# Optimization experiments

Measured on AMD Instinct MI355X. Metric: run time of the kernel, lower is better.

Reference implementation:

```python
import jax, jax.numpy as jnp
import numpy as np

B, S, D, H, INNER = 2, 2048, 1024, 16, 4096
HD = D // H
EPS = 1e-5


def setup_inputs() -> dict:
    key = jax.random.key(0)
    ks = jax.random.split(key, 8)

    def w(k, o, i):
        return jax.random.normal(k, (o, i), jnp.float32) * 0.02

    return {
        "hidden_states": jax.random.normal(ks[0], (B, S, D), jnp.float32),
        "attention_mask": jnp.ones((B, S), jnp.float32),
        "wq": w(ks[1], D, D), "bq": jnp.zeros((D,), jnp.float32),
        "wk": w(ks[2], D, D), "bk": jnp.zeros((D,), jnp.float32),
        "wv": w(ks[3], D, D), "bv": jnp.zeros((D,), jnp.float32),
        "wo": w(ks[4], D, D), "bo": jnp.zeros((D,), jnp.float32),
        "w1": w(ks[5], INNER, D), "b1": jnp.zeros((INNER,), jnp.float32),
        "w2": w(ks[6], D, INNER), "b2": jnp.zeros((D,), jnp.float32),
        "g1": jnp.ones((D,), jnp.float32), "be1": jnp.zeros((D,), jnp.float32),
        "g2": jnp.ones((D,), jnp.float32), "be2": jnp.zeros((D,), jnp.float32),
        "w_bits": 8,
        "a_bits": 8,
    }


def fake_quant(x, bits):
    # symmetric per-tensor fake quantization with straight-through estimator
    qmax = 2.0 ** (bits - 1) - 1.0
    scale = jnp.maximum(jnp.max(jnp.abs(x)), 1e-8) / qmax
    q = jnp.round(jnp.clip(x / scale, -qmax, qmax)) * scale
    return x + jax.lax.stop_gradient(q - x)


def qlinear(x, w, b, w_bits, a_bits):
    return fake_quant(x, a_bits) @ fake_quant(w, w_bits).T + b


def layernorm(x, g, b):
    m = jnp.mean(x, axis=-1, keepdims=True)
    v = jnp.mean((x - m) ** 2, axis=-1, keepdims=True)
    return (x - m) * jax.lax.rsqrt(v + EPS) * g + b


def reference(hidden_states, attention_mask, wq, bq, wk, bk, wv, bv, wo, bo,
              w1, b1, w2, b2, g1, be1, g2, be2, w_bits, a_bits):
    # --- attention sub-block ---
    residual = hidden_states
    x = layernorm(hidden_states, g1, be1)
    q = qlinear(x, wq, bq, w_bits, a_bits).reshape(B, S, H, HD)
    k = qlinear(x, wk, bk, w_bits, a_bits).reshape(B, S, H, HD)
    v = qlinear(x, wv, bv, w_bits, a_bits).reshape(B, S, H, HD)
    scores = jnp.einsum("bqhd,bkhd->bhqk", q, k) / jnp.sqrt(jnp.float32(HD))
    scores = scores + (1.0 - attention_mask)[:, None, None, :] * -10000.0
    probs = jax.nn.softmax(scores, axis=-1)
    attn = jnp.einsum("bhqk,bkhd->bqhd", probs, v).reshape(B, S, D)
    attn = qlinear(attn, wo, bo, w_bits, a_bits)
    hidden = residual + attn
    # --- MLP sub-block ---
    residual = hidden
    x = layernorm(hidden, g2, be2)
    x = qlinear(x, w1, b1, w_bits, a_bits)
    x = jax.nn.gelu(x, approximate=False)
    x = qlinear(x, w2, b2, w_bits, a_bits)
    return residual + x
```

## Files before the change

### kernel.cpp

```cpp
#include <hip/hip_runtime.h>
#include <hip/hip_bf16.h>
#include <math.h>

typedef __bf16 bf16;
typedef signed char i8;
typedef __bf16 bf16x8 __attribute__((ext_vector_type(8)));
typedef __bf16 bf16x4 __attribute__((ext_vector_type(4)));
typedef signed char i8x4 __attribute__((ext_vector_type(4)));
typedef signed char i8x8 __attribute__((ext_vector_type(8)));
typedef int    i32x4 __attribute__((ext_vector_type(4)));
typedef float  f32x4  __attribute__((ext_vector_type(4)));
typedef float  f32x16 __attribute__((ext_vector_type(16)));
typedef unsigned int u32x4 __attribute__((ext_vector_type(4)));

static constexpr int B_  = 2;
static constexpr int S_  = 2048;
static constexpr int D_  = 1024;
static constexpr int H_  = 16;
static constexpr int HD_ = 64;
static constexpr int I_  = 4096;
static constexpr int NT  = B_ * S_;

__device__ __forceinline__ void atomicMaxF(float* p, float v) {
  atomicMax((unsigned int*)p, __float_as_uint(v));
}

__device__ __forceinline__ f32x16 mfma32(bf16x8 a, bf16x8 b, f32x16 c) {
  return __builtin_amdgcn_mfma_f32_32x32x16_bf16(a, b, c, 0, 0, 0);
}

__device__ __forceinline__ i32x4 mfma_i8(i32x4 a, i32x4 b, i32x4 c) {
  return __builtin_amdgcn_mfma_i32_16x16x64_i8(a, b, c, 0, 0, 0);
}

__device__ __forceinline__ void gload16(const void* g, void* lds) {
  __builtin_amdgcn_global_load_lds(
      (const __attribute__((address_space(1))) void*)g,
      (__attribute__((address_space(3))) void*)lds, 16, 0, 0);
}

__device__ __forceinline__ float quant1(float x, float scale, float qmax) {
  return rintf(fminf(fmaxf(x / scale, -qmax), qmax)) * scale;
}
__device__ __forceinline__ i8 quantn(float x, float scale, float qmax) {
  return (i8)(int)rintf(fminf(fmaxf(x / scale, -qmax), qmax));
}

__device__ __forceinline__ void stage64b(const bf16* __restrict__ g, int rs, bf16* lds, int t) {
  #pragma unroll
  for (int r = 0; r < 4; r++) {
    const int cl  = r * 128 + t;
    const int row = cl >> 3;
    const int scr = (cl & 7) ^ (row & 7);
    gload16(g + (size_t)row * rs + scr * 8,
            (char*)lds + (size_t)(r * 128 + (t & 64)) * 16);
  }
}

__global__ __launch_bounds__(256) void k_prep(const float* __restrict__ mask,
                                              float* __restrict__ madd, float* __restrict__ scal) {
  constexpr float MSK2 = -14426.950408889634f;
  const int i = blockIdx.x * 256 + threadIdx.x;
  if (blockIdx.x == 0 && threadIdx.x < 32) scal[threadIdx.x] = 0.f;
  if (i < B_ * S_) madd[i] = (1.0f - mask[i]) * MSK2;
}

struct WArgs {
  const float* w[6];
  i8* q[6];
  size_t n4[6];
};

__global__ __launch_bounds__(256) void k_absmax6(WArgs a, float* __restrict__ slots) {
  const int z = blockIdx.z;
  const float* __restrict__ x = a.w[z];
  const size_t n4 = a.n4[z];
  size_t i = (size_t)blockIdx.x * 256 + threadIdx.x;
  const size_t stride = (size_t)gridDim.x * 256;
  float m = 0.f;
  for (; i < n4; i += stride) {
    float4 v = ((const float4*)x)[i];
    m = fmaxf(m, fmaxf(fmaxf(fabsf(v.x), fabsf(v.y)), fmaxf(fabsf(v.z), fabsf(v.w))));
  }
  #pragma unroll
  for (int o = 32; o; o >>= 1) m = fmaxf(m, __shfl_xor(m, o));
  __shared__ float red[4];
  if ((threadIdx.x & 63) == 0) red[threadIdx.x >> 6] = m;
  __syncthreads();
  if (threadIdx.x == 0)
    atomicMaxF(slots + z, fmaxf(fmaxf(red[0], red[1]), fmaxf(red[2], red[3])));
}

__global__ __launch_bounds__(256) void k_quant6(WArgs a, const float* __restrict__ slots,
                                                const int* __restrict__ bits) {
  const int z = blockIdx.z;
  const float* __restrict__ x = a.w[z];
  i8* __restrict__ y = a.q[z];
  const size_t n4 = a.n4[z];
  const float qmax  = (float)((1 << (*bits - 1)) - 1);
  const float scale = fmaxf(slots[z], 1e-8f) / qmax;
  size_t i = (size_t)blockIdx.x * 256 + threadIdx.x;
  const size_t stride = (size_t)gridDim.x * 256;
  for (; i < n4; i += stride) {
    float4 v = ((const float4*)x)[i];
    i8x4 o;
    o[0] = quantn(v.x, scale, qmax);
    o[1] = quantn(v.y, scale, qmax);
    o[2] = quantn(v.z, scale, qmax);
    o[3] = quantn(v.w, scale, qmax);
    ((i8x4*)y)[i] = o;
  }
}

__global__ __launch_bounds__(256) void k_quant(const float* __restrict__ x, i8* __restrict__ y,
                                               const float* __restrict__ slot,
                                               const int* __restrict__ bits, size_t n4) {
  const float qmax  = (float)((1 << (*bits - 1)) - 1);
  const float scale = fmaxf(*slot, 1e-8f) / qmax;
  size_t i = (size_t)blockIdx.x * 256 + threadIdx.x;
  const size_t stride = (size_t)gridDim.x * 256;
  for (; i < n4; i += stride) {
    float4 v = ((const float4*)x)[i];
    i8x4 o;
    o[0] = quantn(v.x, scale, qmax);
    o[1] = quantn(v.y, scale, qmax);
    o[2] = quantn(v.z, scale, qmax);
    o[3] = quantn(v.w, scale, qmax);
    ((i8x4*)y)[i] = o;
  }
}

__global__ __launch_bounds__(256) void k_qgelu(const bf16* __restrict__ x, i8* __restrict__ y,
                                               const float* __restrict__ slot,
                                               const int* __restrict__ bits, size_t n8) {
  const float qmax  = (float)((1 << (*bits - 1)) - 1);
  const float scale = fmaxf(*slot, 1e-8f) / qmax;
  size_t i = (size_t)blockIdx.x * 256 + threadIdx.x;
  if (i >= n8) return;
  bf16x8 v = ((const bf16x8*)x)[i];
  i8x8 o;
  #pragma unroll
  for (int j = 0; j < 8; j++) o[j] = quantn((float)v[j], scale, qmax);
  ((i8x8*)y)[i] = o;
}

__global__ __launch_bounds__(256) void k_ln(const float* __restrict__ x, const float* __restrict__ g,
                                            const float* __restrict__ be, float* __restrict__ y,
                                            float* __restrict__ slot) {
  const int row = blockIdx.x, t = threadIdx.x;
  const float4 v = ((const float4*)(x + (size_t)row * D_))[t];
  float s = v.x + v.y + v.z + v.w;
  float q = v.x * v.x + v.y * v.y + v.z * v.z + v.w * v.w;
  #pragma unroll
  for (int o = 32; o; o >>= 1) { s += __shfl_xor(s, o); q += __shfl_xor(q, o); }
  __shared__ float red[8];
  const int wid = t >> 6;
  if ((t & 63) == 0) { red[wid] = s; red[4 + wid] = q; }
  __syncthreads();
  s = red[0] + red[1] + red[2] + red[3];
  q = red[4] + red[5] + red[6] + red[7];
  const float mean = s * (1.f / D_);
  const float rstd = rsqrtf(q * (1.f / D_) - mean * mean + 1e-5f);
  const float4 gv = ((const float4*)g)[t];
  const float4 bv = ((const float4*)be)[t];
  float4 o;
  o.x = (v.x - mean) * rstd * gv.x + bv.x;
  o.y = (v.y - mean) * rstd * gv.y + bv.y;
  o.z = (v.z - mean) * rstd * gv.z + bv.z;
  o.w = (v.w - mean) * rstd * gv.w + bv.w;
  ((float4*)(y + (size_t)row * D_))[t] = o;
  float m = fmaxf(fmaxf(fabsf(o.x), fabsf(o.y)), fmaxf(fabsf(o.z), fabsf(o.w)));
  #pragma unroll
  for (int oo = 32; oo; oo >>= 1) m = fmaxf(m, __shfl_xor(m, oo));
  __syncthreads();
  if ((t & 63) == 0) red[wid] = m;
  __syncthreads();
  if (t == 0) atomicMaxF(slot, fmaxf(fmaxf(red[0], red[1]), fmaxf(red[2], red[3])));
}

struct GemmArgs {
  const i8* A;
  const i8* B0; const i8* B1; const i8* B2;
  const float* bias0; const float* bias1; const float* bias2;
  void* out0; void* out1; void* out2;
  const float* res;
  float* slot;
  const float* sa;
  const float* sw0; const float* sw1; const float* sw2;
  const int* abit; const int* wbit;
  int K; int ldc;
};

template <int MODE, int MT>
__device__ __forceinline__ void gemm_body(GemmArgs a, int bx, int by, int bz) {
  constexpr int TM = MT * 32;
  __shared__ __align__(16) i8 As[2][TM * 128];
  __shared__ __align__(16) i8 Bs[2][128 * 128];
  const int t = threadIdx.x, wid = t >> 6, lane = t & 63;
  const int grp = lane >> 4, l15 = lane & 15;
  const int wm = wid >> 1, wn = wid & 1;
  const size_t m0 = (size_t)bx * TM, n0 = (size_t)by * 128;
  const int K = a.K, ldc = a.ldc;

  const i8* Bw; const float* bias; void* outv; const float* swp;
  if constexpr (MODE == 0) {
    Bw   = bz == 0 ? a.B0 : (bz == 1 ? a.B1 : a.B2);
    bias = bz == 0 ? a.bias0 : (bz == 1 ? a.bias1 : a.bias2);
    outv = bz == 0 ? a.out0 : (bz == 1 ? a.out1 : a.out2);
    swp  = bz == 0 ? a.sw0 : (bz == 1 ? a.sw1 : a.sw2);
  } else {
    Bw = a.B0; bias = a.bias0; outv = a.out0; swp = a.sw0;
  }
  const float qa = (float)((1 << (*a.abit - 1)) - 1);
  const float qw = (float)((1 << (*a.wbit - 1)) - 1);
  const float sasw = (fmaxf(*a.sa, 1e-8f) / qa) * (fmaxf(*swp, 1e-8f) / qw);

  i32x4 acc[MT][4];
  #pragma unroll
  for (int m = 0; m < MT; m++)
    #pragma unroll
    for (int n = 0; n < 4; n++) acc[m][n] = i32x4{0, 0, 0, 0};

  auto stage = [&](int kt, int buf) {
    #pragma unroll
    for (int r = 0; r < MT; r++) {
      const int cl = r * 256 + t;
      const int row = cl >> 3, c = cl & 7;
      gload16(a.A + (m0 + row) * (size_t)K + kt + ((c ^ (row & 7)) * 16),
              (char*)&As[buf][0] + (size_t)(r * 256 + (t & 192)) * 16);
    }
    #pragma unroll
    for (int r = 0; r < 4; r++) {
      const int cl = r * 256 + t;
      const int row = cl >> 3, c = cl & 7;
      gload16(Bw + (n0 + row) * (size_t)K + kt + ((c ^ (row & 7)) * 16),
              (char*)&Bs[buf][0] + (size_t)(r * 256 + (t & 192)) * 16);
    }
  };

  stage(0, 0);
  __syncthreads();
  int cur = 0;
  for (int kt = 0; kt < K; kt += 128) {
    if (kt + 128 < K) stage(kt + 128, cur ^ 1);
    #pragma unroll
    for (int ks = 0; ks < 2; ks++) {
      i32x4 bfv[4];
      #pragma unroll
      for (int n = 0; n < 4; n++) {
        const int rb = wn * 64 + n * 16 + l15;
        bfv[n] = *(const i32x4*)(&Bs[cur][0] + rb * 128 + (((ks * 4 + grp) ^ (rb & 7)) * 16));
      }
      #pragma unroll
      for (int m = 0; m < MT; m++) {
        const int ra = wm * (MT * 16) + m * 16 + l15;
        const i32x4 af = *(const i32x4*)(&As[cur][0] + ra * 128 + (((ks * 4 + grp) ^ (ra & 7)) * 16));
        #pragma unroll
        for (int n = 0; n < 4; n++)
          acc[m][n] = mfma_i8(af, bfv[n], acc[m][n]);
      }
    }
    __syncthreads();
    cur ^= 1;
  }

  const size_t gr0 = m0 + wm * (MT * 16) + grp * 4;
  const size_t gc0 = n0 + wn * 64 + l15;

  if constexpr (MODE == 0) {
    if (bz == 2) {
      #pragma unroll
      for (int n = 0; n < 4; n++) {
        const size_t gc = gc0 + n * 16;
        const float bc = bias[gc];
        #pragma unroll
        for (int m = 0; m < MT; m++) {
          const size_t gr = gr0 + m * 16;
          const size_t bb = gr >> 11, s0 = gr & (S_ - 1);
          bf16x4 vv;
          #pragma unroll
          for (int i = 0; i < 4; i++) vv[i] = (bf16)((float)acc[m][n][i] * sasw + bc);
          *(bf16x4*)((bf16*)outv + bb * (size_t)D_ * S_ + gc * S_ + s0) = vv;
        }
      }
      return;
    }
  }

  float lmax = 0.f;
  #pragma unroll
  for (int n = 0; n < 4; n++) {
    const size_t gc = gc0 + n * 16;
    const float bc = bias[gc];
    #pragma unroll
    for (int m = 0; m < MT; m++) {
      const size_t gr = gr0 + m * 16;
      #pragma unroll
      for (int i = 0; i < 4; i++) {
        const float v = (float)acc[m][n][i] * sasw + bc;
        const size_t idx = (gr + i) * (size_t)ldc + gc;
        if constexpr (MODE == 0) {
          ((bf16*)outv)[idx] = (bf16)v;
        } else if constexpr (MODE == 1) {
          ((float*)outv)[idx] = v + a.res[idx];
        } else {
          const float gl = 0.5f * v * (1.0f + erff(v * 0.7071067811865475f));
          ((bf16*)outv)[idx] = (bf16)gl;
          lmax = fmaxf(lmax, fabsf(gl));
        }
      }
    }
  }
  if constexpr (MODE == 2) {
    #pragma unroll
    for (int o = 32; o; o >>= 1) lmax = fmaxf(lmax, __shfl_xor(lmax, o));
    float* red = (float*)&As[0][0];
    if (lane == 0) red[wid] = lmax;
    __syncthreads();
    if (t == 0) atomicMaxF(a.slot, fmaxf(fmaxf(red[0], red[1]), fmaxf(red[2], red[3])));
  }
}

__global__ __launch_bounds__(256) void k_gqkv(GemmArgs a) {
  const int d = blockIdx.x, c = d & 7, s = d >> 3;
  gemm_body<0, 4>(a, s / 3, c, s % 3);
}
__global__ __launch_bounds__(256) void k_gout(GemmArgs a) {
  const int d = blockIdx.x, c = d & 7, s = d >> 3;
  gemm_body<1, 2>(a, s, c, 0);
}
__global__ __launch_bounds__(256) void k_gmlp1(GemmArgs a) {
  const int d = blockIdx.x, c = d & 7, s = d >> 3;
  gemm_body<2, 4>(a, s >> 2, c * 4 + (s & 3), 0);
}
__global__ __launch_bounds__(256) void k_gmlp2(GemmArgs a) {
  const int d = blockIdx.x, c = d & 7, s = d >> 3;
  gemm_body<1, 2>(a, ((c >> 2) << 5) | (s >> 1), ((c & 3) << 1) | (s & 1), 0);
}

__global__ __launch_bounds__(128) void k_attn(const bf16* __restrict__ qb, const bf16* __restrict__ kb,
                                              const bf16* __restrict__ vt, const float* __restrict__ madd,
                                              float* __restrict__ out, float* __restrict__ slot) {
  constexpr float SCL2 = 0.18033688011112042f;
  constexpr float THR  = 8.0f;
  __shared__ __align__(16) bf16 Ks[2][64 * 64];
  __shared__ __align__(16) bf16 Vs[2][64 * 64];
  __shared__ float red[2];
  const int t = threadIdx.x, wid = t >> 6, lane = t & 63;
  const int l31 = lane & 31, hi = lane >> 5;
  const int b = blockIdx.y >> 4, h = blockIdx.y & 15;
  const size_t qkbase = ((size_t)b * S_) * D_ + (size_t)h * HD_;
  const size_t vtbase = (size_t)b * D_ * S_ + (size_t)h * HD_ * S_;
  const int q = blockIdx.x * 64 + wid * 32 + l31;

  bf16x8 qf[4];
  #pragma unroll
  for (int j = 0; j < 4; j++)
    qf[j] = *(const bf16x8*)(qb + qkbase + (size_t)q * D_ + j * 16 + hi * 8);

  f32x16 ao0, ao1;
  #pragma unroll
  for (int r = 0; r < 16; r++) { ao0[r] = 0.f; ao1[r] = 0.f; }
  float mi = -INFINITY, li = 0.f;

  stage64b(kb + qkbase, D_, Ks[0], t);
  stage64b(vt + vtbase, S_, Vs[0], t);
  __syncthreads();
  int cur = 0;

  const float* mp = madd + (size_t)b * S_ + hi * 4;

  for (int kt0 = 0; kt0 < S_; kt0 += 64) {
    f32x4 mv[2][4];
    #pragma unroll
    for (int kb2 = 0; kb2 < 2; kb2++)
      #pragma unroll
      for (int g = 0; g < 4; g++)
        mv[kb2][g] = *(const f32x4*)(mp + kt0 + kb2 * 32 + g * 8);
    __builtin_amdgcn_sched_barrier(0);
    if (kt0 + 64 < S_) {
      stage64b(kb + qkbase + (size_t)(kt0 + 64) * D_, D_, Ks[cur ^ 1], t);
      stage64b(vt + vtbase + (kt0 + 64), S_, Vs[cur ^ 1], t);
    }

    f32x16 s0, s1;
    #pragma unroll
    for (int r = 0; r < 16; r++) { s0[r] = 0.f; s1[r] = 0.f; }
    #pragma unroll
    for (int j = 0; j < 4; j++) {
      const int ch = (j * 2 + hi);
      const bf16x8 kf0 = *(const bf16x8*)(&Ks[cur][0] + l31 * 64 + ((ch ^ (l31 & 7)) * 8));
      const bf16x8 kf1 = *(const bf16x8*)(&Ks[cur][0] + (32 + l31) * 64 + ((ch ^ (l31 & 7)) * 8));
      s0 = mfma32(kf0, qf[j], s0);
      s1 = mfma32(kf1, qf[j], s1);
    }

    float pv_[32];
    #pragma unroll
    for (int r = 0; r < 16; r++) pv_[r]      = s0[r] * SCL2 + mv[0][r >> 2][r & 3];
    #pragma unroll
    for (int r = 0; r < 16; r++) pv_[16 + r] = s1[r] * SCL2 + mv[1][r >> 2][r & 3];

    float mx = pv_[0];
    #pragma unroll
    for (int r = 1; r < 32; r++) mx = fmaxf(mx, pv_[r]);
    mx = fmaxf(mx, __shfl_xor(mx, 32));

    if (!__all(mx - mi <= THR)) {
      const float mnew = fmaxf(mi, mx);
      const float co = exp2f(mi - mnew);
      li *= co;
      #pragma unroll
      for (int r = 0; r < 16; r++) { ao0[r] *= co; ao1[r] *= co; }
      mi = mnew;
    }

    float ls = 0.f;
    #pragma unroll
    for (int r = 0; r < 32; r++) { pv_[r] = exp2f(pv_[r] - mi); ls += pv_[r]; }
    li += ls;

    unsigned pk[16];
    #pragma unroll
    for (int tt = 0; tt < 8; tt++) {
      asm("v_cvt_pk_bf16_f32 %0, %1, %2" : "=v"(pk[tt])     : "v"(pv_[2 * tt]),      "v"(pv_[2 * tt + 1]));
      asm("v_cvt_pk_bf16_f32 %0, %1, %2" : "=v"(pk[8 + tt]) : "v"(pv_[16 + 2 * tt]), "v"(pv_[16 + 2 * tt + 1]));
    }
    #pragma unroll
    for (int g = 0; g < 4; g++) {
      asm volatile("v_permlane32_swap_b32 %0, %1" : "+v"(pk[4 * g]),     "+v"(pk[4 * g + 2]));
      asm volatile("v_permlane32_swap_b32 %0, %1" : "+v"(pk[4 * g + 1]), "+v"(pk[4 * g + 3]));
    }

    #pragma unroll
    for (int j = 0; j < 4; j++) {
      const u32x4 w = {pk[4 * j], pk[4 * j + 1], pk[4 * j + 2], pk[4 * j + 3]};
      const bf16x8 pf = __builtin_bit_cast(bf16x8, w);
      const int ch = (j * 2 + hi);
      const bf16x8 vf0 = *(const bf16x8*)(&Vs[cur][0] + l31 * 64 + ((ch ^ (l31 & 7)) * 8));
      const bf16x8 vf1 = *(const bf16x8*)(&Vs[cur][0] + (32 + l31) * 64 + ((ch ^ (l31 & 7)) * 8));
      ao0 = mfma32(vf0, pf, ao0);
      ao1 = mfma32(vf1, pf, ao1);
    }
    __syncthreads();
    cur ^= 1;
  }

  li += __shfl_xor(li, 32);
  const float invl = 1.0f / li;
  float lmax = 0.f;
  float* orow = out + qkbase + (size_t)q * D_;
  #pragma unroll
  for (int db2 = 0; db2 < 2; db2++) {
    #pragma unroll
    for (int rg = 0; rg < 4; rg++) {
      float4 o;
      o.x = (db2 ? ao1[rg * 4 + 0] : ao0[rg * 4 + 0]) * invl;
      o.y = (db2 ? ao1[rg * 4 + 1] : ao0[rg * 4 + 1]) * invl;
      o.z = (db2 ? ao1[rg * 4 + 2] : ao0[rg * 4 + 2]) * invl;
      o.w = (db2 ? ao1[rg * 4 + 3] : ao0[rg * 4 + 3]) * invl;
      *(float4*)(orow + db2 * 32 + rg * 8 + hi * 4) = o;
      lmax = fmaxf(lmax, fmaxf(fmaxf(fabsf(o.x), fabsf(o.y)), fmaxf(fabsf(o.z), fabsf(o.w))));
    }
  }
  #pragma unroll
  for (int o = 32; o; o >>= 1) lmax = fmaxf(lmax, __shfl_xor(lmax, o));
  if (lane == 0) red[wid] = lmax;
  __syncthreads();
  if (t == 0) atomicMaxF(slot, fmaxf(red[0], red[1]));
}

extern "C" void kernel_launch(void* const* d_in, const int* in_sizes, int n_in,
                              void* d_out, int out_size, void* d_ws, size_t ws_size,
                              hipStream_t stream) {
  const float* hs   = (const float*)d_in[0];
  const float* mask = (const float*)d_in[1];
  const float* wq = (const float*)d_in[2];  const float* bq = (const float*)d_in[3];
  const float* wk = (const float*)d_in[4];  const float* bk = (const float*)d_in[5];
  const float* wv = (const float*)d_in[6];  const float* bv = (const float*)d_in[7];
  const float* wo = (const float*)d_in[8];  const float* bo = (const float*)d_in[9];
  const float* w1 = (const float*)d_in[10]; const float* b1 = (const float*)d_in[11];
  const float* w2 = (const float*)d_in[12]; const float* b2 = (const float*)d_in[13];
  const float* g1 = (const float*)d_in[14]; const float* be1 = (const float*)d_in[15];
  const float* g2 = (const float*)d_in[16]; const float* be2 = (const float*)d_in[17];
  const int* wbits = (const int*)d_in[18];
  const int* abits = (const int*)d_in[19];

  char* ws = (char*)d_ws;
  size_t off = 0;
  float* scal = (float*)ws;                      off += 256;
  float* maddg= (float*)(ws + off);              off += (size_t)NT * 4;
  float* fbuf = (float*)(ws + off);              off += (size_t)NT * D_ * 4;
  i8*    qx   = (i8*)(ws + off);                 off += (size_t)NT * D_;
  bf16*  qb   = (bf16*)(ws + off);               off += (size_t)NT * D_ * 2;
  bf16*  kbuf = (bf16*)(ws + off);               off += (size_t)NT * D_ * 2;
  bf16*  vbuf = (bf16*)(ws + off);               off += (size_t)NT * D_ * 2;
  float* h2   = (float*)(ws + off);              off += (size_t)NT * D_ * 4;
  bf16*  h1   = (bf16*)(ws + off);               off += (size_t)NT * I_ * 2;
  i8*    h1q  = (i8*)(ws + off);                 off += (size_t)NT * I_;
  i8*    wqq  = (i8*)(ws + off);                 off += (size_t)D_ * D_;
  i8*    wkq  = (i8*)(ws + off);                 off += (size_t)D_ * D_;
  i8*    wvq  = (i8*)(ws + off);                 off += (size_t)D_ * D_;
  i8*    woq  = (i8*)(ws + off);                 off += (size_t)D_ * D_;
  i8*    w1q  = (i8*)(ws + off);                 off += (size_t)I_ * D_;
  i8*    w2q  = (i8*)(ws + off);                 off += (size_t)D_ * I_;
  if (ws_size < off) return;

  k_prep<<<NT / 256, 256, 0, stream>>>(mask, maddg, scal);

  const size_t nDD4 = (size_t)D_ * D_ / 4, nDI4 = (size_t)D_ * I_ / 4;
  WArgs wa;
  wa.w[0] = wq; wa.w[1] = wk; wa.w[2] = wv; wa.w[3] = wo; wa.w[4] = w1; wa.w[5] = w2;
  wa.q[0] = wqq; wa.q[1] = wkq; wa.q[2] = wvq; wa.q[3] = woq; wa.q[4] = w1q; wa.q[5] = w2q;
  wa.n4[0] = nDD4; wa.n4[1] = nDD4; wa.n4[2] = nDD4; wa.n4[3] = nDD4;
  wa.n4[4] = nDI4; wa.n4[5] = nDI4;
  k_absmax6<<<dim3(1024, 1, 6), 256, 0, stream>>>(wa, scal + 4);
  k_quant6<<<dim3(1024, 1, 6), 256, 0, stream>>>(wa, scal + 4, wbits);

  const size_t nND4 = (size_t)NT * D_ / 4;

  k_ln<<<NT, 256, 0, stream>>>(hs, g1, be1, fbuf, scal + 0);
  k_quant<<<2048, 256, 0, stream>>>(fbuf, qx, scal + 0, abits, nND4);
  {
    GemmArgs ga{};
    ga.A = qx; ga.B0 = wqq; ga.B1 = wkq; ga.B2 = wvq;
    ga.bias0 = bq; ga.bias1 = bk; ga.bias2 = bv;
    ga.out0 = qb; ga.out1 = kbuf; ga.out2 = vbuf;
    ga.sa = scal + 0; ga.sw0 = scal + 4; ga.sw1 = scal + 5; ga.sw2 = scal + 6;
    ga.abit = abits; ga.wbit = wbits;
    ga.K = D_; ga.ldc = D_;
    k_gqkv<<<(NT / 128) * (D_ / 128) * 3, 256, 0, stream>>>(ga);
  }

  k_attn<<<dim3(S_ / 64, B_ * H_), 128, 0, stream>>>(qb, kbuf, vbuf, maddg, fbuf, scal + 1);
  k_quant<<<2048, 256, 0, stream>>>(fbuf, qx, scal + 1, abits, nND4);
  {
    GemmArgs ga{};
    ga.A = qx; ga.B0 = woq; ga.bias0 = bo; ga.out0 = h2; ga.res = hs;
    ga.sa = scal + 1; ga.sw0 = scal + 7;
    ga.abit = abits; ga.wbit = wbits;
    ga.K = D_; ga.ldc = D_;
    k_gout<<<(NT / 64) * (D_ / 128), 256, 0, stream>>>(ga);
  }

  k_ln<<<NT, 256, 0, stream>>>(h2, g2, be2, fbuf, scal + 2);
  k_quant<<<2048, 256, 0, stream>>>(fbuf, qx, scal + 2, abits, nND4);
  {
    GemmArgs ga{};
    ga.A = qx; ga.B0 = w1q; ga.bias0 = b1; ga.out0 = h1; ga.slot = scal + 3;
    ga.sa = scal + 2; ga.sw0 = scal + 8;
    ga.abit = abits; ga.wbit = wbits;
    ga.K = D_; ga.ldc = I_;
    k_gmlp1<<<(NT / 128) * (I_ / 128), 256, 0, stream>>>(ga);
  }
  k_qgelu<<<(NT * (size_t)I_ / 8 + 255) / 256, 256, 0, stream>>>(h1, h1q, scal + 3, abits,
                                                                 (size_t)NT * I_ / 8);
  {
    GemmArgs ga{};
    ga.A = h1q; ga.B0 = w2q; ga.bias0 = b2; ga.out0 = d_out; ga.res = h2;
    ga.sa = scal + 3; ga.sw0 = scal + 9;
    ga.abit = abits; ga.wbit = wbits;
    ga.K = I_; ga.ldc = D_;
    k_gmlp2<<<(NT / 64) * (D_ / 128), 256, 0, stream>>>(ga);
  }
}
```

Baseline: 427.2 us.

## Split attention over KV halves with combine kernel; deepen GEMM prefetch pipeline

```diff
diff --git a/kernel.cpp b/kernel.cpp
--- a/kernel.cpp
+++ b/kernel.cpp
@@ -46,14 +46,14 @@
   return (i8)(int)rintf(fminf(fmaxf(x / scale, -qmax), qmax));
 }
 
-__device__ __forceinline__ void stage64b(const bf16* __restrict__ g, int rs, bf16* lds, int t) {
-  #pragma unroll
-  for (int r = 0; r < 4; r++) {
-    const int cl  = r * 128 + t;
+__device__ __forceinline__ void stage64(const bf16* __restrict__ g, int rs, bf16* lds, int tt) {
+  #pragma unroll
+  for (int r = 0; r < 2; r++) {
+    const int cl  = r * 256 + tt;
     const int row = cl >> 3;
     const int scr = (cl & 7) ^ (row & 7);
     gload16(g + (size_t)row * rs + scr * 8,
-            (char*)lds + (size_t)(r * 128 + (t & 64)) * 16);
+            (char*)lds + (size_t)(r * 256 + (tt & 192)) * 16);
   }
 }
 
@@ -194,6 +194,7 @@
 template <int MODE, int MT>
 __device__ __forceinline__ void gemm_body(GemmArgs a, int bx, int by, int bz) {
   constexpr int TM = MT * 32;
+  constexpr int NLOAD = MT + 4;
   __shared__ __align__(16) i8 As[2][TM * 128];
   __shared__ __align__(16) i8 Bs[2][128 * 128];
   const int t = threadIdx.x, wid = t >> 6, lane = t & 63;
@@ -211,9 +212,6 @@
   } else {
     Bw = a.B0; bias = a.bias0; outv = a.out0; swp = a.sw0;
   }
-  const float qa = (float)((1 << (*a.abit - 1)) - 1);
-  const float qw = (float)((1 << (*a.wbit - 1)) - 1);
-  const float sasw = (fmaxf(*a.sa, 1e-8f) / qa) * (fmaxf(*swp, 1e-8f) / qw);
 
   i32x4 acc[MT][4];
   #pragma unroll
@@ -239,10 +237,17 @@
   };
 
   stage(0, 0);
-  __syncthreads();
+  if (K > 128) stage(128, 1);
   int cur = 0;
   for (int kt = 0; kt < K; kt += 128) {
-    if (kt + 128 < K) stage(kt + 128, cur ^ 1);
+    if (kt + 128 < K) {
+      if constexpr (MT == 4) asm volatile("s_waitcnt vmcnt(8)" ::: "memory");
+      else                   asm volatile("s_waitcnt vmcnt(6)" ::: "memory");
+    } else {
+      asm volatile("s_waitcnt vmcnt(0)" ::: "memory");
+    }
+    __builtin_amdgcn_sched_barrier(0);
+    __builtin_amdgcn_s_barrier();
     #pragma unroll
     for (int ks = 0; ks < 2; ks++) {
       i32x4 bfv[4];
@@ -260,9 +265,14 @@
           acc[m][n] = mfma_i8(af, bfv[n], acc[m][n]);
       }
     }
-    __syncthreads();
+    __builtin_amdgcn_s_barrier();
+    if (kt + 256 < K) stage(kt + 256, cur);
     cur ^= 1;
   }
+
+  const float qa = (float)((1 << (*a.abit - 1)) - 1);
+  const float qw = (float)((1 << (*a.wbit - 1)) - 1);
+  const float sasw = (fmaxf(*a.sa, 1e-8f) / qa) * (fmaxf(*swp, 1e-8f) / qw);
 
   const size_t gr0 = m0 + wm * (MT * 16) + grp * 4;
   const size_t gc0 = n0 + wn * 64 + l15;
@@ -338,20 +348,21 @@
   gemm_body<1, 2>(a, ((c >> 2) << 5) | (s >> 1), ((c & 3) << 1) | (s & 1), 0);
 }
 
-__global__ __launch_bounds__(128) void k_attn(const bf16* __restrict__ qb, const bf16* __restrict__ kb,
+__global__ __launch_bounds__(256) void k_attn(const bf16* __restrict__ qb, const bf16* __restrict__ kb,
                                               const bf16* __restrict__ vt, const float* __restrict__ madd,
-                                              float* __restrict__ out, float* __restrict__ slot) {
+                                              float* __restrict__ pO, float* __restrict__ ml) {
   constexpr float SCL2 = 0.18033688011112042f;
   constexpr float THR  = 8.0f;
   __shared__ __align__(16) bf16 Ks[2][64 * 64];
   __shared__ __align__(16) bf16 Vs[2][64 * 64];
-  __shared__ float red[2];
   const int t = threadIdx.x, wid = t >> 6, lane = t & 63;
   const int l31 = lane & 31, hi = lane >> 5;
-  const int b = blockIdx.y >> 4, h = blockIdx.y & 15;
+  const int bh = blockIdx.y, b = bh >> 4, h = bh & 15;
+  const int z = blockIdx.z;
+  const int k0base = z * (S_ / 2);
   const size_t qkbase = ((size_t)b * S_) * D_ + (size_t)h * HD_;
   const size_t vtbase = (size_t)b * D_ * S_ + (size_t)h * HD_ * S_;
-  const int q = blockIdx.x * 64 + wid * 32 + l31;
+  const int q = blockIdx.x * 128 + wid * 32 + l31;
 
   bf16x8 qf[4];
   #pragma unroll
@@ -363,14 +374,15 @@
   for (int r = 0; r < 16; r++) { ao0[r] = 0.f; ao1[r] = 0.f; }
   float mi = -INFINITY, li = 0.f;
 
-  stage64b(kb + qkbase, D_, Ks[0], t);
-  stage64b(vt + vtbase, S_, Vs[0], t);
+  stage64(kb + qkbase + (size_t)k0base * D_, D_, Ks[0], t);
+  stage64(vt + vtbase + k0base, S_, Vs[0], t);
   __syncthreads();
   int cur = 0;
 
   const float* mp = madd + (size_t)b * S_ + hi * 4;
 
-  for (int kt0 = 0; kt0 < S_; kt0 += 64) {
+  for (int i = 0; i < S_ / 128; i++) {
+    const int kt0 = k0base + i * 64;
     f32x4 mv[2][4];
     #pragma unroll
     for (int kb2 = 0; kb2 < 2; kb2++)
@@ -378,9 +390,9 @@
       for (int g = 0; g < 4; g++)
         mv[kb2][g] = *(const f32x4*)(mp + kt0 + kb2 * 32 + g * 8);
     __builtin_amdgcn_sched_barrier(0);
-    if (kt0 + 64 < S_) {
-      stage64b(kb + qkbase + (size_t)(kt0 + 64) * D_, D_, Ks[cur ^ 1], t);
-      stage64b(vt + vtbase + (kt0 + 64), S_, Vs[cur ^ 1], t);
+    if (i + 1 < S_ / 128) {
+      stage64(kb + qkbase + (size_t)(kt0 + 64) * D_, D_, Ks[cur ^ 1], t);
+      stage64(vt + vtbase + (kt0 + 64), S_, Vs[cur ^ 1], t);
     }
 
     f32x16 s0, s1;
@@ -447,27 +459,51 @@
   }
 
   li += __shfl_xor(li, 32);
-  const float invl = 1.0f / li;
-  float lmax = 0.f;
-  float* orow = out + qkbase + (size_t)q * D_;
+  const size_t prow = ((size_t)(z * 32 + bh) * S_ + q) * 64;
   #pragma unroll
   for (int db2 = 0; db2 < 2; db2++) {
     #pragma unroll
     for (int rg = 0; rg < 4; rg++) {
       float4 o;
-      o.x = (db2 ? ao1[rg * 4 + 0] : ao0[rg * 4 + 0]) * invl;
-      o.y = (db2 ? ao1[rg * 4 + 1] : ao0[rg * 4 + 1]) * invl;
-      o.z = (db2 ? ao1[rg * 4 + 2] : ao0[rg * 4 + 2]) * invl;
-      o.w = (db2 ? ao1[rg * 4 + 3] : ao0[rg * 4 + 3]) * invl;
-      *(float4*)(orow + db2 * 32 + rg * 8 + hi * 4) = o;
-      lmax = fmaxf(lmax, fmaxf(fmaxf(fabsf(o.x), fabsf(o.y)), fmaxf(fabsf(o.z), fabsf(o.w))));
-    }
-  }
-  #pragma unroll
-  for (int o = 32; o; o >>= 1) lmax = fmaxf(lmax, __shfl_xor(lmax, o));
-  if (lane == 0) red[wid] = lmax;
+      o.x = db2 ? ao1[rg * 4 + 0] : ao0[rg * 4 + 0];
+      o.y = db2 ? ao1[rg * 4 + 1] : ao0[rg * 4 + 1];
+      o.z = db2 ? ao1[rg * 4 + 2] : ao0[rg * 4 + 2];
+      o.w = db2 ? ao1[rg * 4 + 3] : ao0[rg * 4 + 3];
+      *(float4*)(pO + prow + db2 * 32 + rg * 8 + hi * 4) = o;
+    }
+  }
+  if (hi == 0)
+    ((float2*)ml)[(size_t)(z * 32 + bh) * S_ + q] = make_float2(mi, li);
+}
+
+__global__ __launch_bounds__(256) void k_comb(const float* __restrict__ pO,
+                                              const float* __restrict__ ml,
+                                              float* __restrict__ out, float* __restrict__ slot) {
+  const size_t i = (size_t)blockIdx.x * 256 + threadIdx.x;
+  const int d4 = (int)(i & 15);
+  const size_t r = i >> 4;
+  const int bh = (int)(r >> 11), s = (int)(r & (S_ - 1));
+  const int b = bh >> 4, h = bh & 15;
+  const float2 a0 = ((const float2*)ml)[r];
+  const float2 a1 = ((const float2*)ml)[(size_t)32 * S_ + r];
+  const float M = fmaxf(a0.x, a1.x);
+  float w0 = exp2f(a0.x - M), w1 = exp2f(a1.x - M);
+  const float inv = 1.0f / (a0.y * w0 + a1.y * w1);
+  w0 *= inv; w1 *= inv;
+  const f32x4 o0 = ((const f32x4*)pO)[r * 16 + d4];
+  const f32x4 o1 = ((const f32x4*)pO)[(size_t)32 * S_ * 16 + r * 16 + d4];
+  f32x4 o;
+  #pragma unroll
+  for (int j = 0; j < 4; j++) o[j] = o0[j] * w0 + o1[j] * w1;
+  ((f32x4*)out)[(((size_t)(b * S_ + s) * D_ + h * 64) >> 2) + d4] = o;
+  float m = fmaxf(fmaxf(fabsf(o[0]), fabsf(o[1])), fmaxf(fabsf(o[2]), fabsf(o[3])));
+  #pragma unroll
+  for (int oo = 32; oo; oo >>= 1) m = fmaxf(m, __shfl_xor(m, oo));
+  __shared__ float red[4];
+  if ((threadIdx.x & 63) == 0) red[threadIdx.x >> 6] = m;
   __syncthreads();
-  if (t == 0) atomicMaxF(slot, fmaxf(red[0], red[1]));
+  if (threadIdx.x == 0)
+    atomicMaxF(slot, fmaxf(fmaxf(red[0], red[1]), fmaxf(red[2], red[3])));
 }
 
 extern "C" void kernel_launch(void* const* d_in, const int* in_sizes, int n_in,
@@ -498,6 +534,7 @@
   float* h2   = (float*)(ws + off);              off += (size_t)NT * D_ * 4;
   bf16*  h1   = (bf16*)(ws + off);               off += (size_t)NT * I_ * 2;
   i8*    h1q  = (i8*)(ws + off);                 off += (size_t)NT * I_;
+  float* mlb  = (float*)(ws + off);              off += (size_t)2 * 32 * S_ * 8;
   i8*    wqq  = (i8*)(ws + off);                 off += (size_t)D_ * D_;
   i8*    wkq  = (i8*)(ws + off);                 off += (size_t)D_ * D_;
   i8*    wvq  = (i8*)(ws + off);                 off += (size_t)D_ * D_;
@@ -505,6 +542,7 @@
   i8*    w1q  = (i8*)(ws + off);                 off += (size_t)I_ * D_;
   i8*    w2q  = (i8*)(ws + off);                 off += (size_t)D_ * I_;
   if (ws_size < off) return;
+  float* pO = (float*)h1;
 
   k_prep<<<NT / 256, 256, 0, stream>>>(mask, maddg, scal);
 
@@ -532,7 +570,8 @@
     k_gqkv<<<(NT / 128) * (D_ / 128) * 3, 256, 0, stream>>>(ga);
   }
 
-  k_attn<<<dim3(S_ / 64, B_ * H_), 128, 0, stream>>>(qb, kbuf, vbuf, maddg, fbuf, scal + 1);
+  k_attn<<<dim3(S_ / 128, B_ * H_, 2), 256, 0, stream>>>(qb, kbuf, vbuf, maddg, pO, mlb);
+  k_comb<<<(NT * D_ / 4) / 256, 256, 0, stream>>>(pO, mlb, fbuf, scal + 1);
   k_quant<<<2048, 256, 0, stream>>>(fbuf, qx, scal + 1, abits, nND4);
   {
     GemmArgs ga{};
```

After: 471.0 us. 10.3% more time.

## Fuse LayerNorm with activation quantization via cooperative grid sync

Applied to the files above, without the earlier changes.

```diff
diff --git a/kernel.cpp b/kernel.cpp
--- a/kernel.cpp
+++ b/kernel.cpp
@@ -1,6 +1,9 @@
 #include <hip/hip_runtime.h>
 #include <hip/hip_bf16.h>
+#include <hip/hip_cooperative_groups.h>
 #include <math.h>
+
+namespace cg = cooperative_groups;
 
 typedef __bf16 bf16;
 typedef signed char i8;
@@ -39,9 +42,6 @@
       (__attribute__((address_space(3))) void*)lds, 16, 0, 0);
 }
 
-__device__ __forceinline__ float quant1(float x, float scale, float qmax) {
-  return rintf(fminf(fmaxf(x / scale, -qmax), qmax)) * scale;
-}
 __device__ __forceinline__ i8 quantn(float x, float scale, float qmax) {
   return (i8)(int)rintf(fminf(fmaxf(x / scale, -qmax), qmax));
 }
@@ -144,38 +144,58 @@
   ((i8x8*)y)[i] = o;
 }
 
-__global__ __launch_bounds__(256) void k_ln(const float* __restrict__ x, const float* __restrict__ g,
-                                            const float* __restrict__ be, float* __restrict__ y,
-                                            float* __restrict__ slot) {
-  const int row = blockIdx.x, t = threadIdx.x;
-  const float4 v = ((const float4*)(x + (size_t)row * D_))[t];
-  float s = v.x + v.y + v.z + v.w;
-  float q = v.x * v.x + v.y * v.y + v.z * v.z + v.w * v.w;
-  #pragma unroll
-  for (int o = 32; o; o >>= 1) { s += __shfl_xor(s, o); q += __shfl_xor(q, o); }
+__global__ __launch_bounds__(256) void k_lnq(const float* __restrict__ x, const float* __restrict__ g,
+                                             const float* __restrict__ be, i8* __restrict__ y,
+                                             float* __restrict__ slot, const int* __restrict__ bits) {
+  const int t = threadIdx.x;
+  const int row0 = blockIdx.x * 4;
   __shared__ float red[8];
-  const int wid = t >> 6;
-  if ((t & 63) == 0) { red[wid] = s; red[4 + wid] = q; }
-  __syncthreads();
-  s = red[0] + red[1] + red[2] + red[3];
-  q = red[4] + red[5] + red[6] + red[7];
-  const float mean = s * (1.f / D_);
-  const float rstd = rsqrtf(q * (1.f / D_) - mean * mean + 1e-5f);
   const float4 gv = ((const float4*)g)[t];
   const float4 bv = ((const float4*)be)[t];
-  float4 o;
-  o.x = (v.x - mean) * rstd * gv.x + bv.x;
-  o.y = (v.y - mean) * rstd * gv.y + bv.y;
-  o.z = (v.z - mean) * rstd * gv.z + bv.z;
-  o.w = (v.w - mean) * rstd * gv.w + bv.w;
-  ((float4*)(y + (size_t)row * D_))[t] = o;
-  float m = fmaxf(fmaxf(fabsf(o.x), fabsf(o.y)), fmaxf(fabsf(o.z), fabsf(o.w)));
-  #pragma unroll
-  for (int oo = 32; oo; oo >>= 1) m = fmaxf(m, __shfl_xor(m, oo));
-  __syncthreads();
-  if ((t & 63) == 0) red[wid] = m;
+  float4 o[4];
+  float lmax = 0.f;
+  #pragma unroll
+  for (int r = 0; r < 4; r++) {
+    const float4 v = ((const float4*)(x + (size_t)(row0 + r) * D_))[t];
+    float s = v.x + v.y + v.z + v.w;
+    float q = v.x * v.x + v.y * v.y + v.z * v.z + v.w * v.w;
+    #pragma unroll
+    for (int oo = 32; oo; oo >>= 1) { s += __shfl_xor(s, oo); q += __shfl_xor(q, oo); }
+    const int wid = t >> 6;
+    if ((t & 63) == 0) { red[wid] = s; red[4 + wid] = q; }
+    __syncthreads();
+    s = red[0] + red[1] + red[2] + red[3];
+    q = red[4] + red[5] + red[6] + red[7];
+    __syncthreads();
+    const float mean = s * (1.f / D_);
+    const float rstd = rsqrtf(q * (1.f / D_) - mean * mean + 1e-5f);
+    o[r].x = (v.x - mean) * rstd * gv.x + bv.x;
+    o[r].y = (v.y - mean) * rstd * gv.y + bv.y;
+    o[r].z = (v.z - mean) * rstd * gv.z + bv.z;
+    o[r].w = (v.w - mean) * rstd * gv.w + bv.w;
+    lmax = fmaxf(lmax, fmaxf(fmaxf(fabsf(o[r].x), fabsf(o[r].y)),
+                             fmaxf(fabsf(o[r].z), fabsf(o[r].w))));
+  }
+  #pragma unroll
+  for (int oo = 32; oo; oo >>= 1) lmax = fmaxf(lmax, __shfl_xor(lmax, oo));
+  if ((t & 63) == 0) red[t >> 6] = lmax;
   __syncthreads();
   if (t == 0) atomicMaxF(slot, fmaxf(fmaxf(red[0], red[1]), fmaxf(red[2], red[3])));
+  __threadfence();
+  cg::this_grid().sync();
+  if (t == 0) red[0] = __uint_as_float(atomicMax((unsigned int*)slot, 0u));
+  __syncthreads();
+  const float qmax  = (float)((1 << (*bits - 1)) - 1);
+  const float scale = fmaxf(red[0], 1e-8f) / qmax;
+  #pragma unroll
+  for (int r = 0; r < 4; r++) {
+    i8x4 c;
+    c[0] = quantn(o[r].x, scale, qmax);
+    c[1] = quantn(o[r].y, scale, qmax);
+    c[2] = quantn(o[r].z, scale, qmax);
+    c[3] = quantn(o[r].w, scale, qmax);
+    ((i8x4*)(y + (size_t)(row0 + r) * D_))[t] = c;
+  }
 }
 
 struct GemmArgs {
@@ -519,8 +539,12 @@
 
   const size_t nND4 = (size_t)NT * D_ / 4;
 
-  k_ln<<<NT, 256, 0, stream>>>(hs, g1, be1, fbuf, scal + 0);
-  k_quant<<<2048, 256, 0, stream>>>(fbuf, qx, scal + 0, abits, nND4);
+  {
+    const float* x_ = hs; const float* g_ = g1; const float* b_ = be1;
+    i8* y_ = qx; float* s_ = scal + 0; const int* bits_ = abits;
+    void* ka[] = {&x_, &g_, &b_, &y_, &s_, &bits_};
+    hipLaunchCooperativeKernel((void*)k_lnq, dim3(NT / 4), dim3(256), ka, 0, stream);
+  }
   {
     GemmArgs ga{};
     ga.A = qx; ga.B0 = wqq; ga.B1 = wkq; ga.B2 = wvq;
@@ -543,8 +567,12 @@
     k_gout<<<(NT / 64) * (D_ / 128), 256, 0, stream>>>(ga);
   }
 
-  k_ln<<<NT, 256, 0, stream>>>(h2, g2, be2, fbuf, scal + 2);
-  k_quant<<<2048, 256, 0, stream>>>(fbuf, qx, scal + 2, abits, nND4);
+  {
+    const float* x_ = h2; const float* g_ = g2; const float* b_ = be2;
+    i8* y_ = qx; float* s_ = scal + 2; const int* bits_ = abits;
+    void* ka[] = {&x_, &g_, &b_, &y_, &s_, &bits_};
+    hipLaunchCooperativeKernel((void*)k_lnq, dim3(NT / 4), dim3(256), ka, 0, stream);
+  }
   {
     GemmArgs ga{};
     ga.A = qx; ga.B0 = w1q; ga.bias0 = b1; ga.out0 = h1; ga.slot = scal + 3;
```

Measured after the change: 544.4 us. +27.4%, slower.
